# Performance work log

Measured on AMD Instinct MI355X. Metric: run time of the kernel, lower is better.

## Reference

```python
import jax, jax.numpy as jnp
import numpy as np
from jax import lax

H = 64    # enc_hidden_size == dec_hidden_size
IN = 3    # input_size


def gru_cell(x, h, Wih, Whh, bih, bhh):
    """PyTorch-style GRU cell. x:[N,in], h:[N,H]."""
    gi = x @ Wih.T + bih
    gh = h @ Whh.T + bhh
    ir, iz, inn = jnp.split(gi, 3, axis=-1)
    hr, hz, hn = jnp.split(gh, 3, axis=-1)
    r = jax.nn.sigmoid(ir + hr)
    z = jax.nn.sigmoid(iz + hz)
    n = jnp.tanh(inn + r * hn)
    return (1.0 - z) * n + z * h


def setup_inputs():
    key = jax.random.key(0)
    ks = jax.random.split(key, 20)
    B, S, A = 128, 100, 32
    s = 0.05
    w = lambda k, shape: (jax.random.normal(k, shape, dtype=jnp.float32) * s)
    inp = {}
    inp["src"] = jax.random.normal(ks[0], (B, S, A * IN), dtype=jnp.float32)
    # encoder (bidirectional, 1 layer)
    inp["enc_Wih_f"] = w(ks[1], (3 * H, IN))
    inp["enc_Whh_f"] = w(ks[2], (3 * H, H))
    inp["enc_bih_f"] = w(ks[3], (3 * H,))
    inp["enc_bhh_f"] = w(ks[4], (3 * H,))
    inp["enc_Wih_b"] = w(ks[5], (3 * H, IN))
    inp["enc_Whh_b"] = w(ks[6], (3 * H, H))
    inp["enc_bih_b"] = w(ks[7], (3 * H,))
    inp["enc_bhh_b"] = w(ks[8], (3 * H,))
    # attention: Linear(2H + H -> H), v: Linear(H -> 1, no bias)
    inp["attn_W"] = w(ks[9], (H, 3 * H))
    inp["attn_b"] = w(ks[10], (H,))
    inp["attn_v"] = w(ks[11], (H,))
    # enc_to_dec: Linear(2H -> H)
    inp["e2d_W"] = w(ks[12], (H, 2 * H))
    inp["e2d_b"] = w(ks[13], (H,))
    # decoder GRU: input = IN + 2H
    inp["dec_Wih"] = w(ks[14], (3 * H, IN + 2 * H))
    inp["dec_Whh"] = w(ks[15], (3 * H, H))
    inp["dec_bih"] = w(ks[16], (3 * H,))
    inp["dec_bhh"] = w(ks[17], (3 * H,))
    # fc_out: Linear(H -> IN)
    inp["out_W"] = w(ks[18], (IN, H))
    inp["out_b"] = w(ks[19], (IN,))
    inp["pred_len"] = 12
    return inp


def reference(src, enc_Wih_f, enc_Whh_f, enc_bih_f, enc_bhh_f,
              enc_Wih_b, enc_Whh_b, enc_bih_b, enc_bhh_b,
              attn_W, attn_b, attn_v, e2d_W, e2d_b,
              dec_Wih, dec_Whh, dec_bih, dec_bhh, out_W, out_b, pred_len):
    B, S, F = src.shape
    A = F // IN
    N = B * A
    # Agents share all weights -> fold agent dim into batch (same math as the
    # original per-agent Python loop).
    x = src.reshape(B, S, A, IN).transpose(0, 2, 1, 3).reshape(N, S, IN)
    xs = x.transpose(1, 0, 2)  # [S, N, IN]
    h0 = jnp.zeros((N, H), dtype=src.dtype)

    def step_f(h, xt):
        h = gru_cell(xt, h, enc_Wih_f, enc_Whh_f, enc_bih_f, enc_bhh_f)
        return h, h

    def step_b(h, xt):
        h = gru_cell(xt, h, enc_Wih_b, enc_Whh_b, enc_bih_b, enc_bhh_b)
        return h, h

    hf, outs_f = lax.scan(step_f, h0, xs)
    hb, outs_b = lax.scan(step_b, h0, xs[::-1])
    enc_out = jnp.concatenate([outs_f, outs_b[::-1]], axis=-1).transpose(1, 0, 2)  # [N,S,2H]
    hidden_cat = jnp.concatenate([hf, hb], axis=-1)  # [N, 2H]
    h_dec0 = hidden_cat @ e2d_W.T + e2d_b            # [N, H]
    dec_in0 = x[:, -1, :]                            # [N, IN]

    def dec_step(carry, _):
        h, inp = carry
        # Bahdanau attention over encoder outputs
        hid_rep = jnp.broadcast_to(h[:, None, :], (N, S, H))
        energy = jnp.tanh(jnp.concatenate([hid_rep, enc_out], axis=-1) @ attn_W.T + attn_b)
        score = energy @ attn_v                       # [N, S]
        aw = jax.nn.softmax(score, axis=1)
        context = jnp.einsum('ns,nsd->nd', aw, enc_out)  # [N, 2H]
        rnn_in = jnp.concatenate([inp, context], axis=-1)  # [N, IN+2H]
        h = gru_cell(rnn_in, h, dec_Wih, dec_Whh, dec_bih, dec_bhh)
        pred = h @ out_W.T + out_b                    # [N, IN]
        return (h, pred), pred

    (_, _), preds = lax.scan(dec_step, (h_dec0, dec_in0), None, length=pred_len)
    # preds: [P, N, IN] -> [B, P, A*IN]
    out = preds.transpose(1, 0, 2).reshape(B, A, pred_len, IN).transpose(0, 2, 1, 3).reshape(B, pred_len, A * IN)
    if pred_len == 1:
        out = out[:, 0, :]
    return out
```

## Files before the change

kernel.cpp:

```cpp
#include <hip/hip_runtime.h>
#include <stdint.h>

#define SLEN 100
#define NSEQ 4096
#define PRED 12

typedef unsigned short ushort_t;
typedef unsigned int uint_t;

#if __has_builtin(__builtin_amdgcn_rcpf)
#define RCP(x) __builtin_amdgcn_rcpf(x)
#else
#define RCP(x) (1.0f/(x))
#endif

__device__ __forceinline__ float bfu(ushort_t u){ return __uint_as_float(((uint_t)u)<<16); }
__device__ __forceinline__ float bflo(uint_t u){ return __uint_as_float(u<<16); }
__device__ __forceinline__ float bfhi(uint_t u){ return __uint_as_float(u & 0xffff0000u); }
__device__ __forceinline__ ushort_t f2bf(float f){
  uint_t u = __float_as_uint(f);
  u += 0x7fffu + ((u>>16)&1u);
  return (ushort_t)(u>>16);
}
__device__ __forceinline__ uint_t pk2(float a, float b){
  return (uint_t)f2bf(a) | ((uint_t)f2bf(b)<<16);
}
__device__ __forceinline__ float fsig(float x){ return RCP(1.f + __expf(-x)); }
__device__ __forceinline__ float ftanh(float x){ float e = __expf(x+x); return 1.f - 2.f*RCP(e+1.f); }

__global__ __launch_bounds__(256, 2)
void k_encoder(const float* __restrict__ src,
               const float* __restrict__ WihF, const float* __restrict__ WhhF,
               const float* __restrict__ bihF, const float* __restrict__ bhhF,
               const float* __restrict__ WihB, const float* __restrict__ WhhB,
               const float* __restrict__ bihB, const float* __restrict__ bhhB,
               ushort_t* __restrict__ encO, float* __restrict__ hlast)
{
  __shared__ __align__(16) float Wrz[64*64*2];
  __shared__ __align__(16) float Wn [64*64];
  __shared__ __align__(16) float hpack[4*64*4];
  __shared__ __align__(16) float xbuf[4][12];

  const int t = threadIdx.x;
  const int dir = blockIdx.x >> 8;
  const int grp = blockIdx.x & 255;
  const float* Wih = dir ? WihB : WihF;
  const float* Whh = dir ? WhhB : WhhF;
  const float* bih = dir ? bihB : bihF;
  const float* bhh = dir ? bhhB : bhhF;

  for (int e = t; e < 12288; e += 256) {
    float v = Whh[e];
    int row = e >> 6, k = e & 63;
    int g = row >> 6, j = row & 63;
    if (g < 2) Wrz[(k*64+j)*2 + g] = v;
    else       Wn[k*64+j] = v;
  }
  const int w = t >> 6, lane = t & 63;
  const int n0 = grp*16 + w*4;

  float rw[3][3];
  #pragma unroll
  for (int g = 0; g < 3; ++g)
    #pragma unroll
    for (int i = 0; i < 3; ++i)
      rw[g][i] = Wih[(g*64 + lane)*3 + i];
  const float br  = bih[lane]     + bhh[lane];
  const float bz  = bih[64+lane]  + bhh[64+lane];
  const float bni = bih[128+lane];
  const float bnh = bhh[128+lane];

  float hreg[4] = {0.f,0.f,0.f,0.f};
  *(float4*)&hpack[(w*64+lane)*4] = make_float4(0.f,0.f,0.f,0.f);
  __syncthreads();

  for (int st = 0; st < SLEN; ++st) {
    const int sidx = dir ? (SLEN-1 - st) : st;
    if (lane < 12) {
      int q = lane/3, i = lane - q*3;
      int n = n0 + q;
      xbuf[w][lane] = src[(((n>>5)*SLEN + sidx)*96) + (n&31)*3 + i];
    }
    __syncthreads();

    float a_r[4], a_z[4], a_n[4], gn[4];
    #pragma unroll
    for (int q = 0; q < 4; ++q) {
      float x0 = xbuf[w][q*3+0], x1 = xbuf[w][q*3+1], x2 = xbuf[w][q*3+2];
      a_r[q] = br  + x0*rw[0][0] + x1*rw[0][1] + x2*rw[0][2];
      a_z[q] = bz  + x0*rw[1][0] + x1*rw[1][1] + x2*rw[1][2];
      gn[q]  = bni + x0*rw[2][0] + x1*rw[2][1] + x2*rw[2][2];
      a_n[q] = bnh;
    }
    #pragma unroll 4
    for (int k = 0; k < 64; ++k) {
      float2 wrz = *(const float2*)&Wrz[(k*64+lane)*2];
      float  wn  = Wn[k*64+lane];
      float4 h4  = *(const float4*)&hpack[(w*64+k)*4];
      a_r[0] += h4.x*wrz.x; a_z[0] += h4.x*wrz.y; a_n[0] += h4.x*wn;
      a_r[1] += h4.y*wrz.x; a_z[1] += h4.y*wrz.y; a_n[1] += h4.y*wn;
      a_r[2] += h4.z*wrz.x; a_z[2] += h4.z*wrz.y; a_n[2] += h4.z*wn;
      a_r[3] += h4.w*wrz.x; a_z[3] += h4.w*wrz.y; a_n[3] += h4.w*wn;
    }
    float4 hnew;
    float* hn = (float*)&hnew;
    #pragma unroll
    for (int q = 0; q < 4; ++q) {
      float r  = fsig(a_r[q]);
      float z  = fsig(a_z[q]);
      float nn = ftanh(gn[q] + r*a_n[q]);
      float hv = nn + z*(hreg[q] - nn);
      hreg[q] = hv; hn[q] = hv;
      encO[((n0+q)*SLEN + sidx)*128 + dir*64 + lane] = f2bf(hv);
    }
    __builtin_amdgcn_wave_barrier();
    *(float4*)&hpack[(w*64+lane)*4] = hnew;
  }
  #pragma unroll
  for (int q = 0; q < 4; ++q)
    hlast[(dir*NSEQ + n0+q)*64 + lane] = hreg[q];
}

__global__ __launch_bounds__(256)
void k_hdec0(const float* __restrict__ hlast, const float* __restrict__ e2dW,
             const float* __restrict__ e2db, float* __restrict__ h0g)
{
  const int t = threadIdx.x, w = t>>6, lane = t&63;
  const int n = blockIdx.x*4 + w;
  const float* hf = hlast + n*64;
  const float* hb = hlast + (NSEQ + n)*64;
  float a0 = e2db[lane], a1 = 0.f;
  #pragma unroll 4
  for (int k = 0; k < 64; k += 2) {
    a0 += hf[k]  *e2dW[lane*128 + k]      + hb[k]  *e2dW[lane*128 + 64 + k];
    a1 += hf[k+1]*e2dW[lane*128 + k + 1]  + hb[k+1]*e2dW[lane*128 + 65 + k];
  }
  h0g[n*64 + lane] = a0 + a1;
}

__global__ __launch_bounds__(512)
void k_encwb(const ushort_t* __restrict__ encO, const float* __restrict__ attnW,
             const float* __restrict__ attnb, ushort_t* __restrict__ encWbG)
{
  __shared__ __align__(16) uint_t encL[96*64];
  __shared__ __align__(16) float  WeT[128*64];
  const int t = threadIdx.x;
  const int row0 = blockIdx.x * 96;
  const int nrows = (409600 - row0) < 96 ? (409600 - row0) : 96;
  const uint_t* srcp = (const uint_t*)(encO) + row0*64;
  for (int e = t; e < nrows*64; e += 512) encL[e] = srcp[e];
  for (int e = t; e < 8192; e += 512) {
    int j = e >> 7, k = e & 127;
    WeT[k*64 + j] = attnW[j*192 + 64 + k];
  }
  __syncthreads();
  const int w = t>>6, lane = t&63;
  const float ab = attnb[lane];
  for (int rr = 0; rr < 12; ++rr) {
    int row = w*12 + rr;
    if (row0 + row >= 409600) break;
    float a0 = ab, a1 = 0.f;
    #pragma unroll 8
    for (int k2 = 0; k2 < 64; ++k2) {
      uint_t u = encL[row*64 + k2];
      a0 += bflo(u)*WeT[(2*k2  )*64 + lane];
      a1 += bfhi(u)*WeT[(2*k2+1)*64 + lane];
    }
    encWbG[(row0+row)*64 + lane] = f2bf(a0 + a1);
  }
}

__global__ __launch_bounds__(256, 2)
void k_decoder(const float* __restrict__ src,
               const ushort_t* __restrict__ encO, const ushort_t* __restrict__ encWbG,
               const float* __restrict__ h0g,
               const float* __restrict__ attnW, const float* __restrict__ attnv,
               const float* __restrict__ dWih, const float* __restrict__ dWhh,
               const float* __restrict__ dbih, const float* __restrict__ dbhh,
               const float* __restrict__ outWg, const float* __restrict__ outbg,
               float* __restrict__ out)
{
  __shared__ __align__(16) ushort_t encBT[128*104];
  __shared__ __align__(16) ushort_t encWbL[100*66];
  __shared__ __align__(16) ushort_t WhT[64*64];
  __shared__ __align__(16) ushort_t WihIs[3*192];
  __shared__ __align__(16) float brz[128];
  __shared__ __align__(16) float bnn[128];
  __shared__ __align__(16) float vat[64];
  __shared__ __align__(16) float outWs[192];
  __shared__ __align__(16) float outbs[4];
  __shared__ __align__(16) float hbuf[64];
  __shared__ __align__(16) float hWb[64];
  __shared__ __align__(16) float score[104];
  __shared__ __align__(16) float ctx[128];
  __shared__ __align__(16) float gbuf[256];
  __shared__ __align__(16) float inpb[4];

  const int t = threadIdx.x;
  const int n = blockIdx.x;

  uint_t wihc[64];
  float  whhf[64];
  if (t < 192) {
    const float* wr = dWih + t*131 + 3;
    #pragma unroll
    for (int kk = 0; kk < 64; ++kk) wihc[kk] = pk2(wr[2*kk], wr[2*kk+1]);
    const float* hr = dWhh + t*64;
    #pragma unroll
    for (int kk = 0; kk < 64; ++kk) whhf[kk] = hr[kk];
  }
  const ushort_t* eb = encO + n*12800;
  for (int e = t; e < 12800; e += 256) {
    int s = e >> 7, k = e & 127;
    encBT[k*104 + s] = eb[e];
  }
  for (int e = t; e < 512; e += 256) {
    int k = e >> 2, s = 100 + (e & 3);
    encBT[k*104 + s] = 0;
  }
  const ushort_t* ew = encWbG + n*6400;
  for (int e = t; e < 6400; e += 256) {
    int s = e >> 6, j = e & 63;
    encWbL[s*66 + j] = ew[e];
  }
  for (int e = t; e < 4096; e += 256) {
    int j = e >> 6, k = e & 63;
    WhT[k*64 + j] = f2bf(attnW[j*192 + k]);
  }
  if (t < 192) {
    WihIs[t]       = f2bf(dWih[t*131 + 0]);
    WihIs[192 + t] = f2bf(dWih[t*131 + 1]);
    WihIs[384 + t] = f2bf(dWih[t*131 + 2]);
    outWs[t] = outWg[t];
  }
  if (t < 128) brz[t] = dbih[t] + dbhh[t];
  if (t < 64) { bnn[t] = dbih[128+t]; bnn[64+t] = dbhh[128+t]; vat[t] = attnv[t]; hbuf[t] = h0g[n*64+t]; }
  if (t < 4)  outbs[t] = (t < 3) ? outbg[t] : 0.f;
  if (t < 3)  inpb[t] = src[((n>>5)*SLEN + (SLEN-1))*96 + (n&31)*3 + t];
  if (t >= 100 && t < 104) score[t] = 0.f;
  __syncthreads();

  for (int st = 0; st < PRED; ++st) {
    if (t < 64) {
      float a0 = 0.f, a1 = 0.f;
      #pragma unroll 8
      for (int k = 0; k < 64; k += 2) {
        a0 += hbuf[k]  *bfu(WhT[k*64 + t]);
        a1 += hbuf[k+1]*bfu(WhT[(k+1)*64 + t]);
      }
      hWb[t] = a0 + a1;
    }
    __syncthreads();
    if (t < 200) {
      int s = t % 100, jh = t / 100;
      const ushort_t* erow = &encWbL[s*66 + jh*32];
      float p = 0.f;
      #pragma unroll
      for (int j4 = 0; j4 < 8; ++j4) {
        float4 hw4 = *(const float4*)&hWb[jh*32 + j4*4];
        uint_t u0 = *(const uint_t*)&erow[j4*4];
        uint_t u1 = *(const uint_t*)&erow[j4*4 + 2];
        float4 vv  = *(const float4*)&vat[jh*32 + j4*4];
        p += ftanh(hw4.x + bflo(u0))*vv.x;
        p += ftanh(hw4.y + bfhi(u0))*vv.y;
        p += ftanh(hw4.z + bflo(u1))*vv.z;
        p += ftanh(hw4.w + bfhi(u1))*vv.w;
      }
      gbuf[jh*100 + s] = p;
    }
    __syncthreads();
    if (t < 64) {
      float sA = gbuf[t] + gbuf[100+t];
      float sB = (t < 36) ? (gbuf[64+t] + gbuf[164+t]) : -1e30f;
      float m = fmaxf(sA, sB);
      #pragma unroll
      for (int o = 32; o > 0; o >>= 1) m = fmaxf(m, __shfl_xor(m, o, 64));
      float pA = __expf(sA - m);
      float pB = (t < 36) ? __expf(sB - m) : 0.f;
      float sm = pA + pB;
      #pragma unroll
      for (int o = 32; o > 0; o >>= 1) sm += __shfl_xor(sm, o, 64);
      float inv = RCP(sm);
      score[t] = pA * inv;
      if (t < 36) score[64+t] = pB * inv;
    }
    __syncthreads();
    if (t < 128) {
      const uint_t* rowp = (const uint_t*)&encBT[t*104];
      float a0 = 0.f, a1 = 0.f;
      #pragma unroll 4
      for (int s2 = 0; s2 < 52; ++s2) {
        uint_t u = rowp[s2];
        float2 sc = *(const float2*)&score[s2*2];
        a0 += bflo(u)*sc.x;
        a1 += bfhi(u)*sc.y;
      }
      ctx[t] = a0 + a1;
    }
    __syncthreads();
    if (t < 192) {
      float ai0 = inpb[0]*bfu(WihIs[t]) + inpb[1]*bfu(WihIs[192+t]) + inpb[2]*bfu(WihIs[384+t]);
      float ai1 = 0.f;
      #pragma unroll
      for (int kk = 0; kk < 64; ++kk) {
        uint_t wv = wihc[kk];
        float2 c2 = *(const float2*)&ctx[2*kk];
        ai0 += c2.x*bflo(wv);
        ai1 += c2.y*bfhi(wv);
      }
      float ah = 0.f;
      #pragma unroll
      for (int kk = 0; kk < 64; ++kk) ah += hbuf[kk]*whhf[kk];
      float ai = ai0 + ai1;
      if (t < 128) {
        gbuf[t] = fsig(ai + ah + brz[t]);
      } else {
        int j = t - 128;
        gbuf[128+j] = ai + bnn[j];
        gbuf[192+j] = ah + bnn[64+j];
      }
    }
    __syncthreads();
    if (t < 64) {
      float r = gbuf[t], z = gbuf[64+t];
      float nn = ftanh(gbuf[128+t] + r*gbuf[192+t]);
      float hv = nn + z*(hbuf[t] - nn);
      hbuf[t] = hv;
      float p0 = hv*outWs[t], p1 = hv*outWs[64+t], p2 = hv*outWs[128+t];
      #pragma unroll
      for (int o = 32; o > 0; o >>= 1) {
        p0 += __shfl_xor(p0, o, 64);
        p1 += __shfl_xor(p1, o, 64);
        p2 += __shfl_xor(p2, o, 64);
      }
      if (t < 3) {
        float pv = (t==0) ? p0 : ((t==1) ? p1 : p2);
        pv += outbs[t];
        out[((n>>5)*PRED + st)*96 + (n&31)*3 + t] = pv;
        inpb[t] = pv;
      }
    }
    __syncthreads();
  }
}

extern "C" void kernel_launch(void* const* d_in, const int* in_sizes, int n_in,
                              void* d_out, int out_size, void* d_ws, size_t ws_size,
                              hipStream_t stream)
{
  const float* src   = (const float*)d_in[0];
  const float* WihF  = (const float*)d_in[1];
  const float* WhhF  = (const float*)d_in[2];
  const float* bihF  = (const float*)d_in[3];
  const float* bhhF  = (const float*)d_in[4];
  const float* WihB  = (const float*)d_in[5];
  const float* WhhB  = (const float*)d_in[6];
  const float* bihB  = (const float*)d_in[7];
  const float* bhhB  = (const float*)d_in[8];
  const float* attnW = (const float*)d_in[9];
  const float* attnb = (const float*)d_in[10];
  const float* attnv = (const float*)d_in[11];
  const float* e2dW  = (const float*)d_in[12];
  const float* e2db  = (const float*)d_in[13];
  const float* dWih  = (const float*)d_in[14];
  const float* dWhh  = (const float*)d_in[15];
  const float* dbih  = (const float*)d_in[16];
  const float* dbhh  = (const float*)d_in[17];
  const float* outW  = (const float*)d_in[18];
  const float* outb  = (const float*)d_in[19];

  char* w = (char*)d_ws;
  ushort_t* encO   = (ushort_t*)w;
  ushort_t* encWbG = (ushort_t*)(w + 104857600);
  float*    hlast  = (float*)   (w + 157286400);
  float*    h0g    = (float*)   (w + 159383552);
  float* out = (float*)d_out;

  hipLaunchKernelGGL(k_encoder, dim3(512), dim3(256), 0, stream,
                     src, WihF, WhhF, bihF, bhhF, WihB, WhhB, bihB, bhhB, encO, hlast);
  hipLaunchKernelGGL(k_hdec0, dim3(1024), dim3(256), 0, stream, hlast, e2dW, e2db, h0g);
  hipLaunchKernelGGL(k_encwb, dim3(4267), dim3(512), 0, stream, encO, attnW, attnb, encWbG);
  hipLaunchKernelGGL(k_decoder, dim3(4096), dim3(256), 0, stream,
                     src, encO, encWbG, h0g, attnW, attnv, dWih, dWhh, dbih, dbhh, outW, outb, out);
}
```

Measured before the change: 1.335 ms.

## Halve per-wave sequences in encoder, bf16 weights; move decoder hW into registers

The encoder now gives each wave 2 sequences instead of 4 and launches twice as many blocks (1024), so the serial 100-step recurrence is spread over more waves. Its recurrent weights are stored as bf16 in LDS, shrinking shared memory use. Inputs are now shuffled across lanes instead of staged through LDS with a block-wide syncthreads per step. In the decoder, the attention hidden projection and the Whh matvec run in parallel using register-resident weights (the idle threads 192-255 hold packed attnW), and the encBT padding is trimmed. This trades some precision in the encoder recurrence for shorter per-step latency and more occupancy.

```diff
diff --git a/kernel.cpp b/kernel.cpp
--- a/kernel.cpp
+++ b/kernel.cpp
@@ -36,28 +36,25 @@
                const float* __restrict__ bihB, const float* __restrict__ bhhB,
                ushort_t* __restrict__ encO, float* __restrict__ hlast)
 {
-  __shared__ __align__(16) float Wrz[64*64*2];
-  __shared__ __align__(16) float Wn [64*64];
-  __shared__ __align__(16) float hpack[4*64*4];
-  __shared__ __align__(16) float xbuf[4][12];
+  __shared__ __align__(16) uint_t   Wrzp[64*64];
+  __shared__ __align__(16) ushort_t Wns [64*64];
+  __shared__ __align__(16) float    hpack[4][64][2];
 
   const int t = threadIdx.x;
-  const int dir = blockIdx.x >> 8;
-  const int grp = blockIdx.x & 255;
+  const int dir = blockIdx.x >> 9;
+  const int grp = blockIdx.x & 511;
   const float* Wih = dir ? WihB : WihF;
   const float* Whh = dir ? WhhB : WhhF;
   const float* bih = dir ? bihB : bihF;
   const float* bhh = dir ? bhhB : bhhF;
 
-  for (int e = t; e < 12288; e += 256) {
-    float v = Whh[e];
-    int row = e >> 6, k = e & 63;
-    int g = row >> 6, j = row & 63;
-    if (g < 2) Wrz[(k*64+j)*2 + g] = v;
-    else       Wn[k*64+j] = v;
+  for (int e = t; e < 4096; e += 256) {
+    int j = e & 63, k = e >> 6;
+    Wrzp[k*64 + j] = pk2(Whh[j*64 + k], Whh[(64+j)*64 + k]);
+    Wns [k*64 + j] = f2bf(Whh[(128+j)*64 + k]);
   }
   const int w = t >> 6, lane = t & 63;
-  const int n0 = grp*16 + w*4;
+  const int n0 = grp*8 + w*2;
 
   float rw[3][3];
   #pragma unroll
@@ -70,55 +67,58 @@
   const float bni = bih[128+lane];
   const float bnh = bhh[128+lane];
 
-  float hreg[4] = {0.f,0.f,0.f,0.f};
-  *(float4*)&hpack[(w*64+lane)*4] = make_float4(0.f,0.f,0.f,0.f);
+  float hreg[2] = {0.f,0.f};
+  hpack[w][lane][0] = 0.f; hpack[w][lane][1] = 0.f;
   __syncthreads();
 
   for (int st = 0; st < SLEN; ++st) {
     const int sidx = dir ? (SLEN-1 - st) : st;
-    if (lane < 12) {
+    float xv = 0.f;
+    if (lane < 6) {
       int q = lane/3, i = lane - q*3;
       int n = n0 + q;
-      xbuf[w][lane] = src[(((n>>5)*SLEN + sidx)*96) + (n&31)*3 + i];
-    }
-    __syncthreads();
-
-    float a_r[4], a_z[4], a_n[4], gn[4];
-    #pragma unroll
-    for (int q = 0; q < 4; ++q) {
-      float x0 = xbuf[w][q*3+0], x1 = xbuf[w][q*3+1], x2 = xbuf[w][q*3+2];
-      a_r[q] = br  + x0*rw[0][0] + x1*rw[0][1] + x2*rw[0][2];
-      a_z[q] = bz  + x0*rw[1][0] + x1*rw[1][1] + x2*rw[1][2];
-      gn[q]  = bni + x0*rw[2][0] + x1*rw[2][1] + x2*rw[2][2];
-      a_n[q] = bnh;
-    }
-    #pragma unroll 4
+      xv = src[(((n>>5)*SLEN + sidx)*96) + (n&31)*3 + i];
+    }
+    const float x00 = __shfl(xv, 0, 64), x01 = __shfl(xv, 1, 64), x02 = __shfl(xv, 2, 64);
+    const float x10 = __shfl(xv, 3, 64), x11 = __shfl(xv, 4, 64), x12 = __shfl(xv, 5, 64);
+
+    float a_r0 = br  + x00*rw[0][0] + x01*rw[0][1] + x02*rw[0][2];
+    float a_z0 = bz  + x00*rw[1][0] + x01*rw[1][1] + x02*rw[1][2];
+    float gn0  = bni + x00*rw[2][0] + x01*rw[2][1] + x02*rw[2][2];
+    float a_r1 = br  + x10*rw[0][0] + x11*rw[0][1] + x12*rw[0][2];
+    float a_z1 = bz  + x10*rw[1][0] + x11*rw[1][1] + x12*rw[1][2];
+    float gn1  = bni + x10*rw[2][0] + x11*rw[2][1] + x12*rw[2][2];
+    float a_n0 = bnh, a_n1 = bnh;
+
+    #pragma unroll 8
     for (int k = 0; k < 64; ++k) {
-      float2 wrz = *(const float2*)&Wrz[(k*64+lane)*2];
-      float  wn  = Wn[k*64+lane];
-      float4 h4  = *(const float4*)&hpack[(w*64+k)*4];
-      a_r[0] += h4.x*wrz.x; a_z[0] += h4.x*wrz.y; a_n[0] += h4.x*wn;
-      a_r[1] += h4.y*wrz.x; a_z[1] += h4.y*wrz.y; a_n[1] += h4.y*wn;
-      a_r[2] += h4.z*wrz.x; a_z[2] += h4.z*wrz.y; a_n[2] += h4.z*wn;
-      a_r[3] += h4.w*wrz.x; a_z[3] += h4.w*wrz.y; a_n[3] += h4.w*wn;
-    }
-    float4 hnew;
-    float* hn = (float*)&hnew;
-    #pragma unroll
-    for (int q = 0; q < 4; ++q) {
-      float r  = fsig(a_r[q]);
-      float z  = fsig(a_z[q]);
-      float nn = ftanh(gn[q] + r*a_n[q]);
-      float hv = nn + z*(hreg[q] - nn);
-      hreg[q] = hv; hn[q] = hv;
-      encO[((n0+q)*SLEN + sidx)*128 + dir*64 + lane] = f2bf(hv);
+      uint_t wp = Wrzp[k*64 + lane];
+      float  wr = bflo(wp), wz = bfhi(wp);
+      float  wn = bfu(Wns[k*64 + lane]);
+      float2 h2 = *(const float2*)&hpack[w][k][0];
+      a_r0 += h2.x*wr; a_z0 += h2.x*wz; a_n0 += h2.x*wn;
+      a_r1 += h2.y*wr; a_z1 += h2.y*wz; a_n1 += h2.y*wn;
+    }
+    {
+      float r  = fsig(a_r0);
+      float z  = fsig(a_z0);
+      float nn = ftanh(gn0 + r*a_n0);
+      hreg[0] = nn + z*(hreg[0] - nn);
+      encO[((n0+0)*SLEN + sidx)*128 + dir*64 + lane] = f2bf(hreg[0]);
+    }
+    {
+      float r  = fsig(a_r1);
+      float z  = fsig(a_z1);
+      float nn = ftanh(gn1 + r*a_n1);
+      hreg[1] = nn + z*(hreg[1] - nn);
+      encO[((n0+1)*SLEN + sidx)*128 + dir*64 + lane] = f2bf(hreg[1]);
     }
     __builtin_amdgcn_wave_barrier();
-    *(float4*)&hpack[(w*64+lane)*4] = hnew;
-  }
-  #pragma unroll
-  for (int q = 0; q < 4; ++q)
-    hlast[(dir*NSEQ + n0+q)*64 + lane] = hreg[q];
+    *(float2*)&hpack[w][lane][0] = make_float2(hreg[0], hreg[1]);
+    __builtin_amdgcn_wave_barrier();
+  }
+  hlast[(dir*NSEQ + n0+0)*64 + lane] = hreg[0];
+  hlast[(dir*NSEQ + n0+1)*64 + lane] = hreg[1];
 }
 
 __global__ __launch_bounds__(256)
@@ -180,9 +180,8 @@
                const float* __restrict__ outWg, const float* __restrict__ outbg,
                float* __restrict__ out)
 {
-  __shared__ __align__(16) ushort_t encBT[128*104];
+  __shared__ __align__(16) ushort_t encBT[128*102];
   __shared__ __align__(16) ushort_t encWbL[100*66];
-  __shared__ __align__(16) ushort_t WhT[64*64];
   __shared__ __align__(16) ushort_t WihIs[3*192];
   __shared__ __align__(16) float brz[128];
   __shared__ __align__(16) float bnn[128];
@@ -191,6 +190,7 @@
   __shared__ __align__(16) float outbs[4];
   __shared__ __align__(16) float hbuf[64];
   __shared__ __align__(16) float hWb[64];
+  __shared__ __align__(16) float ahb[192];
   __shared__ __align__(16) float score[104];
   __shared__ __align__(16) float ctx[128];
   __shared__ __align__(16) float gbuf[256];
@@ -208,24 +208,24 @@
     const float* hr = dWhh + t*64;
     #pragma unroll
     for (int kk = 0; kk < 64; ++kk) whhf[kk] = hr[kk];
+  } else {
+    const int j = t - 192;
+    #pragma unroll
+    for (int kk = 0; kk < 32; ++kk) wihc[kk] = pk2(attnW[j*192 + 2*kk], attnW[j*192 + 2*kk + 1]);
   }
   const ushort_t* eb = encO + n*12800;
   for (int e = t; e < 12800; e += 256) {
     int s = e >> 7, k = e & 127;
-    encBT[k*104 + s] = eb[e];
-  }
-  for (int e = t; e < 512; e += 256) {
-    int k = e >> 2, s = 100 + (e & 3);
-    encBT[k*104 + s] = 0;
+    encBT[k*102 + s] = eb[e];
+  }
+  if (t < 256) {
+    int k = t >> 1, s = 100 + (t & 1);
+    encBT[k*102 + s] = 0;
   }
   const ushort_t* ew = encWbG + n*6400;
   for (int e = t; e < 6400; e += 256) {
     int s = e >> 6, j = e & 63;
     encWbL[s*66 + j] = ew[e];
-  }
-  for (int e = t; e < 4096; e += 256) {
-    int j = e >> 6, k = e & 63;
-    WhT[k*64 + j] = f2bf(attnW[j*192 + k]);
   }
   if (t < 192) {
     WihIs[t]       = f2bf(dWih[t*131 + 0]);
@@ -241,14 +241,19 @@
   __syncthreads();
 
   for (int st = 0; st < PRED; ++st) {
-    if (t < 64) {
-      float a0 = 0.f, a1 = 0.f;
-      #pragma unroll 8
-      for (int k = 0; k < 64; k += 2) {
-        a0 += hbuf[k]  *bfu(WhT[k*64 + t]);
-        a1 += hbuf[k+1]*bfu(WhT[(k+1)*64 + t]);
-      }
-      hWb[t] = a0 + a1;
+    if (t < 192) {
+      float ah = 0.f;
+      #pragma unroll
+      for (int kk = 0; kk < 64; ++kk) ah += hbuf[kk]*whhf[kk];
+      ahb[t] = ah;
+    } else {
+      float a = 0.f;
+      #pragma unroll
+      for (int kk = 0; kk < 32; ++kk) {
+        uint_t wv = wihc[kk];
+        a += hbuf[2*kk]*bflo(wv) + hbuf[2*kk+1]*bfhi(wv);
+      }
+      hWb[t - 192] = a;
     }
     __syncthreads();
     if (t < 200) {
@@ -286,10 +291,10 @@
     }
     __syncthreads();
     if (t < 128) {
-      const uint_t* rowp = (const uint_t*)&encBT[t*104];
+      const uint_t* rowp = (const uint_t*)&encBT[t*102];
       float a0 = 0.f, a1 = 0.f;
       #pragma unroll 4
-      for (int s2 = 0; s2 < 52; ++s2) {
+      for (int s2 = 0; s2 < 51; ++s2) {
         uint_t u = rowp[s2];
         float2 sc = *(const float2*)&score[s2*2];
         a0 += bflo(u)*sc.x;
@@ -308,10 +313,7 @@
         ai0 += c2.x*bflo(wv);
         ai1 += c2.y*bfhi(wv);
       }
-      float ah = 0.f;
-      #pragma unroll
-      for (int kk = 0; kk < 64; ++kk) ah += hbuf[kk]*whhf[kk];
-      float ai = ai0 + ai1;
+      float ai = ai0 + ai1, ah = ahb[t];
       if (t < 128) {
         gbuf[t] = fsig(ai + ah + brz[t]);
       } else {
@@ -376,7 +378,7 @@
   float*    h0g    = (float*)   (w + 159383552);
   float* out = (float*)d_out;
 
-  hipLaunchKernelGGL(k_encoder, dim3(512), dim3(256), 0, stream,
+  hipLaunchKernelGGL(k_encoder, dim3(1024), dim3(256), 0, stream,
                      src, WihF, WhhF, bihF, bhhF, WihB, WhhB, bihB, bhhB, encO, hlast);
   hipLaunchKernelGGL(k_hdec0, dim3(1024), dim3(256), 0, stream, hlast, e2dW, e2db, h0g);
   hipLaunchKernelGGL(k_encwb, dim3(4267), dim3(512), 0, stream, encO, attnW, attnb, encWbG);
```

Result: slower. 1.501 ms (+12.5%).

## Move encoder weights into registers with readlane broadcast; restructure decoder syncs

Applied to the files above, without the earlier changes.

The encoder keeps the recurrent weights as packed bf16 in registers instead of LDS and broadcasts hidden state with readlane, so the per-step block barrier goes away and the next input is prefetched. The decoder computes the attention hidden projection redundantly per wave from register weights and moves the Whh matvec earlier to overlap. It also fuses softmax and context into per-wave work, removing two block barriers per step, and shrinks LDS so launch bounds can target three blocks per CU. The cost is more register pressure and reduced precision of encoder Whh, now bf16.

```diff
diff --git a/kernel.cpp b/kernel.cpp
--- a/kernel.cpp
+++ b/kernel.cpp
@@ -27,6 +27,9 @@
 }
 __device__ __forceinline__ float fsig(float x){ return RCP(1.f + __expf(-x)); }
 __device__ __forceinline__ float ftanh(float x){ float e = __expf(x+x); return 1.f - 2.f*RCP(e+1.f); }
+__device__ __forceinline__ float RL(float v, int k){
+  return __uint_as_float((uint_t)__builtin_amdgcn_readlane((int)__float_as_uint(v), k));
+}
 
 __global__ __launch_bounds__(256, 2)
 void k_encoder(const float* __restrict__ src,
@@ -36,11 +39,6 @@
                const float* __restrict__ bihB, const float* __restrict__ bhhB,
                ushort_t* __restrict__ encO, float* __restrict__ hlast)
 {
-  __shared__ __align__(16) float Wrz[64*64*2];
-  __shared__ __align__(16) float Wn [64*64];
-  __shared__ __align__(16) float hpack[4*64*4];
-  __shared__ __align__(16) float xbuf[4][12];
-
   const int t = threadIdx.x;
   const int dir = blockIdx.x >> 8;
   const int grp = blockIdx.x & 255;
@@ -49,15 +47,16 @@
   const float* bih = dir ? bihB : bihF;
   const float* bhh = dir ? bhhB : bhhF;
 
-  for (int e = t; e < 12288; e += 256) {
-    float v = Whh[e];
-    int row = e >> 6, k = e & 63;
-    int g = row >> 6, j = row & 63;
-    if (g < 2) Wrz[(k*64+j)*2 + g] = v;
-    else       Wn[k*64+j] = v;
-  }
   const int w = t >> 6, lane = t & 63;
   const int n0 = grp*16 + w*4;
+
+  uint_t wrz[64], wn2[32];
+  #pragma unroll
+  for (int k = 0; k < 64; ++k)
+    wrz[k] = pk2(Whh[lane*64 + k], Whh[(64+lane)*64 + k]);
+  #pragma unroll
+  for (int kk = 0; kk < 32; ++kk)
+    wn2[kk] = pk2(Whh[(128+lane)*64 + 2*kk], Whh[(128+lane)*64 + 2*kk+1]);
 
   float rw[3][3];
   #pragma unroll
@@ -70,55 +69,86 @@
   const float bni = bih[128+lane];
   const float bnh = bhh[128+lane];
 
-  float hreg[4] = {0.f,0.f,0.f,0.f};
-  *(float4*)&hpack[(w*64+lane)*4] = make_float4(0.f,0.f,0.f,0.f);
-  __syncthreads();
+  float h0=0.f, h1=0.f, h2=0.f, h3=0.f;
+
+  float xv = 0.f;
+  {
+    const int s0 = dir ? (SLEN-1) : 0;
+    if (lane < 12) {
+      int q = lane/3, i = lane - q*3, n = n0 + q;
+      xv = src[(((n>>5)*SLEN + s0)*96) + (n&31)*3 + i];
+    }
+  }
 
   for (int st = 0; st < SLEN; ++st) {
     const int sidx = dir ? (SLEN-1 - st) : st;
-    if (lane < 12) {
-      int q = lane/3, i = lane - q*3;
-      int n = n0 + q;
-      xbuf[w][lane] = src[(((n>>5)*SLEN + sidx)*96) + (n&31)*3 + i];
-    }
-    __syncthreads();
-
-    float a_r[4], a_z[4], a_n[4], gn[4];
+    const float x00=RL(xv,0),  x01=RL(xv,1),  x02=RL(xv,2);
+    const float x10=RL(xv,3),  x11=RL(xv,4),  x12=RL(xv,5);
+    const float x20=RL(xv,6),  x21=RL(xv,7),  x22=RL(xv,8);
+    const float x30=RL(xv,9),  x31=RL(xv,10), x32=RL(xv,11);
+    float xnx = 0.f;
+    if (st+1 < SLEN) {
+      const int sn = dir ? (SLEN-2 - st) : (st+1);
+      if (lane < 12) {
+        int q = lane/3, i = lane - q*3, n = n0 + q;
+        xnx = src[(((n>>5)*SLEN + sn)*96) + (n&31)*3 + i];
+      }
+    }
+
+    float ar0 = br  + x00*rw[0][0] + x01*rw[0][1] + x02*rw[0][2];
+    float az0 = bz  + x00*rw[1][0] + x01*rw[1][1] + x02*rw[1][2];
+    float gn0 = bni + x00*rw[2][0] + x01*rw[2][1] + x02*rw[2][2];
+    float ar1 = br  + x10*rw[0][0] + x11*rw[0][1] + x12*rw[0][2];
+    float az1 = bz  + x10*rw[1][0] + x11*rw[1][1] + x12*rw[1][2];
+    float gn1 = bni + x10*rw[2][0] + x11*rw[2][1] + x12*rw[2][2];
+    float ar2 = br  + x20*rw[0][0] + x21*rw[0][1] + x22*rw[0][2];
+    float az2 = bz  + x20*rw[1][0] + x21*rw[1][1] + x22*rw[1][2];
+    float gn2 = bni + x20*rw[2][0] + x21*rw[2][1] + x22*rw[2][2];
+    float ar3 = br  + x30*rw[0][0] + x31*rw[0][1] + x32*rw[0][2];
+    float az3 = bz  + x30*rw[1][0] + x31*rw[1][1] + x32*rw[1][2];
+    float gn3 = bni + x30*rw[2][0] + x31*rw[2][1] + x32*rw[2][2];
+    float an0 = bnh, an1 = bnh, an2 = bnh, an3 = bnh;
+
     #pragma unroll
-    for (int q = 0; q < 4; ++q) {
-      float x0 = xbuf[w][q*3+0], x1 = xbuf[w][q*3+1], x2 = xbuf[w][q*3+2];
-      a_r[q] = br  + x0*rw[0][0] + x1*rw[0][1] + x2*rw[0][2];
-      a_z[q] = bz  + x0*rw[1][0] + x1*rw[1][1] + x2*rw[1][2];
-      gn[q]  = bni + x0*rw[2][0] + x1*rw[2][1] + x2*rw[2][2];
-      a_n[q] = bnh;
-    }
-    #pragma unroll 4
     for (int k = 0; k < 64; ++k) {
-      float2 wrz = *(const float2*)&Wrz[(k*64+lane)*2];
-      float  wn  = Wn[k*64+lane];
-      float4 h4  = *(const float4*)&hpack[(w*64+k)*4];
-      a_r[0] += h4.x*wrz.x; a_z[0] += h4.x*wrz.y; a_n[0] += h4.x*wn;
-      a_r[1] += h4.y*wrz.x; a_z[1] += h4.y*wrz.y; a_n[1] += h4.y*wn;
-      a_r[2] += h4.z*wrz.x; a_z[2] += h4.z*wrz.y; a_n[2] += h4.z*wn;
-      a_r[3] += h4.w*wrz.x; a_z[3] += h4.w*wrz.y; a_n[3] += h4.w*wn;
-    }
-    float4 hnew;
-    float* hn = (float*)&hnew;
-    #pragma unroll
-    for (int q = 0; q < 4; ++q) {
-      float r  = fsig(a_r[q]);
-      float z  = fsig(a_z[q]);
-      float nn = ftanh(gn[q] + r*a_n[q]);
-      float hv = nn + z*(hreg[q] - nn);
-      hreg[q] = hv; hn[q] = hv;
-      encO[((n0+q)*SLEN + sidx)*128 + dir*64 + lane] = f2bf(hv);
-    }
-    __builtin_amdgcn_wave_barrier();
-    *(float4*)&hpack[(w*64+lane)*4] = hnew;
-  }
-  #pragma unroll
-  for (int q = 0; q < 4; ++q)
-    hlast[(dir*NSEQ + n0+q)*64 + lane] = hreg[q];
+      const float hk0 = RL(h0,k), hk1 = RL(h1,k), hk2 = RL(h2,k), hk3 = RL(h3,k);
+      const float wr_ = bflo(wrz[k]), wz_ = bfhi(wrz[k]);
+      const float wn_ = (k & 1) ? bfhi(wn2[k>>1]) : bflo(wn2[k>>1]);
+      ar0 += hk0*wr_; az0 += hk0*wz_; an0 += hk0*wn_;
+      ar1 += hk1*wr_; az1 += hk1*wz_; an1 += hk1*wn_;
+      ar2 += hk2*wr_; az2 += hk2*wz_; an2 += hk2*wn_;
+      ar3 += hk3*wr_; az3 += hk3*wz_; an3 += hk3*wn_;
+    }
+    {
+      float r = fsig(ar0), z = fsig(az0);
+      float nn = ftanh(gn0 + r*an0);
+      h0 = nn + z*(h0 - nn);
+      encO[((n0+0)*SLEN + sidx)*128 + dir*64 + lane] = f2bf(h0);
+    }
+    {
+      float r = fsig(ar1), z = fsig(az1);
+      float nn = ftanh(gn1 + r*an1);
+      h1 = nn + z*(h1 - nn);
+      encO[((n0+1)*SLEN + sidx)*128 + dir*64 + lane] = f2bf(h1);
+    }
+    {
+      float r = fsig(ar2), z = fsig(az2);
+      float nn = ftanh(gn2 + r*an2);
+      h2 = nn + z*(h2 - nn);
+      encO[((n0+2)*SLEN + sidx)*128 + dir*64 + lane] = f2bf(h2);
+    }
+    {
+      float r = fsig(ar3), z = fsig(az3);
+      float nn = ftanh(gn3 + r*an3);
+      h3 = nn + z*(h3 - nn);
+      encO[((n0+3)*SLEN + sidx)*128 + dir*64 + lane] = f2bf(h3);
+    }
+    xv = xnx;
+  }
+  hlast[(dir*NSEQ + n0+0)*64 + lane] = h0;
+  hlast[(dir*NSEQ + n0+1)*64 + lane] = h1;
+  hlast[(dir*NSEQ + n0+2)*64 + lane] = h2;
+  hlast[(dir*NSEQ + n0+3)*64 + lane] = h3;
 }
 
 __global__ __launch_bounds__(256)
@@ -170,7 +200,7 @@
   }
 }
 
-__global__ __launch_bounds__(256, 2)
+__global__ __launch_bounds__(256, 3)
 void k_decoder(const float* __restrict__ src,
                const ushort_t* __restrict__ encO, const ushort_t* __restrict__ encWbG,
                const float* __restrict__ h0g,
@@ -180,118 +210,119 @@
                const float* __restrict__ outWg, const float* __restrict__ outbg,
                float* __restrict__ out)
 {
-  __shared__ __align__(16) ushort_t encBT[128*104];
+  __shared__ __align__(16) ushort_t encBT[128*102];
   __shared__ __align__(16) ushort_t encWbL[100*66];
-  __shared__ __align__(16) ushort_t WhT[64*64];
-  __shared__ __align__(16) ushort_t WihIs[3*192];
-  __shared__ __align__(16) float brz[128];
-  __shared__ __align__(16) float bnn[128];
+  __shared__ __align__(16) float hWw[4][64];
+  __shared__ __align__(16) float scoreW[2][104];
+  __shared__ __align__(16) float ctx[128];
+  __shared__ __align__(16) float gbuf[256];
+  __shared__ __align__(16) float hbuf[64];
   __shared__ __align__(16) float vat[64];
   __shared__ __align__(16) float outWs[192];
   __shared__ __align__(16) float outbs[4];
-  __shared__ __align__(16) float hbuf[64];
-  __shared__ __align__(16) float hWb[64];
-  __shared__ __align__(16) float score[104];
-  __shared__ __align__(16) float ctx[128];
-  __shared__ __align__(16) float gbuf[256];
   __shared__ __align__(16) float inpb[4];
 
   const int t = threadIdx.x;
   const int n = blockIdx.x;
+  const int w = t >> 6, lane = t & 63;
 
   uint_t wihc[64];
-  float  whhf[64];
+  uint_t whh2[32];
+  uint_t whp[32];
+  float  wx0=0.f, wx1=0.f, wx2=0.f;
+  float  brz_r=0.f, bni_r=0.f, bnh_r=0.f;
+  #pragma unroll
+  for (int kk = 0; kk < 32; ++kk)
+    whp[kk] = pk2(attnW[lane*192 + 2*kk], attnW[lane*192 + 2*kk + 1]);
   if (t < 192) {
     const float* wr = dWih + t*131 + 3;
     #pragma unroll
     for (int kk = 0; kk < 64; ++kk) wihc[kk] = pk2(wr[2*kk], wr[2*kk+1]);
     const float* hr = dWhh + t*64;
     #pragma unroll
-    for (int kk = 0; kk < 64; ++kk) whhf[kk] = hr[kk];
+    for (int kk = 0; kk < 32; ++kk) whh2[kk] = pk2(hr[2*kk], hr[2*kk+1]);
+    wx0 = dWih[t*131 + 0]; wx1 = dWih[t*131 + 1]; wx2 = dWih[t*131 + 2];
+    if (t < 128) brz_r = dbih[t] + dbhh[t];
+    else { bni_r = dbih[t]; bnh_r = dbhh[t]; }
   }
   const ushort_t* eb = encO + n*12800;
   for (int e = t; e < 12800; e += 256) {
     int s = e >> 7, k = e & 127;
-    encBT[k*104 + s] = eb[e];
-  }
-  for (int e = t; e < 512; e += 256) {
-    int k = e >> 2, s = 100 + (e & 3);
-    encBT[k*104 + s] = 0;
+    encBT[k*102 + s] = eb[e];
   }
   const ushort_t* ew = encWbG + n*6400;
   for (int e = t; e < 6400; e += 256) {
     int s = e >> 6, j = e & 63;
     encWbL[s*66 + j] = ew[e];
   }
-  for (int e = t; e < 4096; e += 256) {
-    int j = e >> 6, k = e & 63;
-    WhT[k*64 + j] = f2bf(attnW[j*192 + k]);
-  }
-  if (t < 192) {
-    WihIs[t]       = f2bf(dWih[t*131 + 0]);
-    WihIs[192 + t] = f2bf(dWih[t*131 + 1]);
-    WihIs[384 + t] = f2bf(dWih[t*131 + 2]);
-    outWs[t] = outWg[t];
-  }
-  if (t < 128) brz[t] = dbih[t] + dbhh[t];
-  if (t < 64) { bnn[t] = dbih[128+t]; bnn[64+t] = dbhh[128+t]; vat[t] = attnv[t]; hbuf[t] = h0g[n*64+t]; }
+  if (t < 192) outWs[t] = outWg[t];
+  if (t < 64) { vat[t] = attnv[t]; hbuf[t] = h0g[n*64+t]; }
   if (t < 4)  outbs[t] = (t < 3) ? outbg[t] : 0.f;
   if (t < 3)  inpb[t] = src[((n>>5)*SLEN + (SLEN-1))*96 + (n&31)*3 + t];
-  if (t >= 100 && t < 104) score[t] = 0.f;
   __syncthreads();
 
   for (int st = 0; st < PRED; ++st) {
-    if (t < 64) {
-      float a0 = 0.f, a1 = 0.f;
-      #pragma unroll 8
-      for (int k = 0; k < 64; k += 2) {
-        a0 += hbuf[k]  *bfu(WhT[k*64 + t]);
-        a1 += hbuf[k+1]*bfu(WhT[(k+1)*64 + t]);
-      }
-      hWb[t] = a0 + a1;
+    {
+      float hw = 0.f;
+      #pragma unroll
+      for (int kk = 0; kk < 32; ++kk) {
+        float2 h2 = *(const float2*)&hbuf[2*kk];
+        uint_t u = whp[kk];
+        hw += h2.x*bflo(u) + h2.y*bfhi(u);
+      }
+      hWw[w][lane] = hw;
+    }
+    float ah = 0.f;
+    if (t < 192) {
+      #pragma unroll
+      for (int kk = 0; kk < 32; ++kk) {
+        float2 h2 = *(const float2*)&hbuf[2*kk];
+        uint_t u = whh2[kk];
+        ah += h2.x*bflo(u) + h2.y*bfhi(u);
+      }
+    }
+    __builtin_amdgcn_wave_barrier();
+    {
+      const int s = t & 127, jh = t >> 7;
+      if (s < 100) {
+        const ushort_t* erow = &encWbL[s*66 + jh*32];
+        float p = 0.f;
+        #pragma unroll
+        for (int j4 = 0; j4 < 8; ++j4) {
+          float4 hw4 = *(const float4*)&hWw[w][jh*32 + j4*4];
+          uint_t u0 = *(const uint_t*)&erow[j4*4];
+          uint_t u1 = *(const uint_t*)&erow[j4*4 + 2];
+          float4 vv = *(const float4*)&vat[jh*32 + j4*4];
+          p += ftanh(hw4.x + bflo(u0))*vv.x;
+          p += ftanh(hw4.y + bfhi(u0))*vv.y;
+          p += ftanh(hw4.z + bflo(u1))*vv.z;
+          p += ftanh(hw4.w + bfhi(u1))*vv.w;
+        }
+        gbuf[t] = p;
+      }
     }
     __syncthreads();
-    if (t < 200) {
-      int s = t % 100, jh = t / 100;
-      const ushort_t* erow = &encWbL[s*66 + jh*32];
-      float p = 0.f;
-      #pragma unroll
-      for (int j4 = 0; j4 < 8; ++j4) {
-        float4 hw4 = *(const float4*)&hWb[jh*32 + j4*4];
-        uint_t u0 = *(const uint_t*)&erow[j4*4];
-        uint_t u1 = *(const uint_t*)&erow[j4*4 + 2];
-        float4 vv  = *(const float4*)&vat[jh*32 + j4*4];
-        p += ftanh(hw4.x + bflo(u0))*vv.x;
-        p += ftanh(hw4.y + bfhi(u0))*vv.y;
-        p += ftanh(hw4.z + bflo(u1))*vv.z;
-        p += ftanh(hw4.w + bfhi(u1))*vv.w;
-      }
-      gbuf[jh*100 + s] = p;
-    }
-    __syncthreads();
-    if (t < 64) {
-      float sA = gbuf[t] + gbuf[100+t];
-      float sB = (t < 36) ? (gbuf[64+t] + gbuf[164+t]) : -1e30f;
+    if (t < 128) {
+      float sA = gbuf[lane] + gbuf[128+lane];
+      float sB = (lane < 36) ? (gbuf[64+lane] + gbuf[192+lane]) : -1e30f;
       float m = fmaxf(sA, sB);
       #pragma unroll
       for (int o = 32; o > 0; o >>= 1) m = fmaxf(m, __shfl_xor(m, o, 64));
       float pA = __expf(sA - m);
-      float pB = (t < 36) ? __expf(sB - m) : 0.f;
+      float pB = (lane < 36) ? __expf(sB - m) : 0.f;
       float sm = pA + pB;
       #pragma unroll
       for (int o = 32; o > 0; o >>= 1) sm += __shfl_xor(sm, o, 64);
       float inv = RCP(sm);
-      score[t] = pA * inv;
-      if (t < 36) score[64+t] = pB * inv;
-    }
-    __syncthreads();
-    if (t < 128) {
-      const uint_t* rowp = (const uint_t*)&encBT[t*104];
+      scoreW[w][lane] = pA * inv;
+      if (lane < 36) scoreW[w][64+lane] = pB * inv;
+      __builtin_amdgcn_wave_barrier();
+      const uint_t* rowp = (const uint_t*)&encBT[t*102];
       float a0 = 0.f, a1 = 0.f;
-      #pragma unroll 4
-      for (int s2 = 0; s2 < 52; ++s2) {
+      #pragma unroll 5
+      for (int s2 = 0; s2 < 50; ++s2) {
         uint_t u = rowp[s2];
-        float2 sc = *(const float2*)&score[s2*2];
+        float2 sc = *(const float2*)&scoreW[w][2*s2];
         a0 += bflo(u)*sc.x;
         a1 += bfhi(u)*sc.y;
       }
@@ -299,7 +330,7 @@
     }
     __syncthreads();
     if (t < 192) {
-      float ai0 = inpb[0]*bfu(WihIs[t]) + inpb[1]*bfu(WihIs[192+t]) + inpb[2]*bfu(WihIs[384+t]);
+      float ai0 = inpb[0]*wx0 + inpb[1]*wx1 + inpb[2]*wx2;
       float ai1 = 0.f;
       #pragma unroll
       for (int kk = 0; kk < 64; ++kk) {
@@ -308,17 +339,9 @@
         ai0 += c2.x*bflo(wv);
         ai1 += c2.y*bfhi(wv);
       }
-      float ah = 0.f;
-      #pragma unroll
-      for (int kk = 0; kk < 64; ++kk) ah += hbuf[kk]*whhf[kk];
       float ai = ai0 + ai1;
-      if (t < 128) {
-        gbuf[t] = fsig(ai + ah + brz[t]);
-      } else {
-        int j = t - 128;
-        gbuf[128+j] = ai + bnn[j];
-        gbuf[192+j] = ah + bnn[64+j];
-      }
+      if (t < 128) gbuf[t] = fsig(ai + ah + brz_r);
+      else { gbuf[t] = ai + bni_r; gbuf[64+t] = ah + bnh_r; }
     }
     __syncthreads();
     if (t < 64) {
```

After: 4.085 ms. 3.06x slower.
